# Performance work log

Measured on AMD Instinct MI355X. Metric: run time of the kernel, lower is better.

## Reference

```python
import jax, jax.numpy as jnp
import numpy as np

N, E, D_IN, H, D_OUT = 65536, 8, 90, 256, 4
MARGIN = 2.0  # boundary_margin
EPS = 1e-8


def setup_inputs() -> dict:
    key = jax.random.key(0)
    ks = jax.random.split(key, 6)
    return {
        "x": jax.random.normal(ks[0], (N, 3 + D_IN), dtype=jnp.float32),
        "centroids": jax.random.normal(ks[1], (E, 3), dtype=jnp.float32),
        "W1": jax.random.normal(ks[2], (E, D_IN, H), dtype=jnp.float32) * 0.05,
        "b1": jnp.zeros((E, H), dtype=jnp.float32),
        "W2": jax.random.normal(ks[3], (E, H, H), dtype=jnp.float32) * 0.05,
        "b2": jnp.zeros((E, H), dtype=jnp.float32),
        "W3": jax.random.normal(ks[4], (E, H, D_OUT), dtype=jnp.float32) * 0.05,
        "b3": jnp.zeros((E, D_OUT), dtype=jnp.float32),
    }


def _routing_weights(xyz, centroids):
    # torch.cdist(x[:, :3], centroids): Euclidean distance [N, E]
    diff = xyz[:, None, :] - centroids[None, :, :]
    d = jnp.sqrt(jnp.sum(diff * diff, axis=-1))
    inv = 1.0 / (d + EPS)
    dmin = jnp.min(d, axis=1, keepdims=True)
    inv = jnp.where(d > MARGIN * dmin, 0.0, inv)  # zero out far clusters
    return inv / jnp.sum(inv, axis=-1, keepdims=True)  # [N, E]


def reference(x, centroids, W1, b1, W2, b2, W3, b3):
    w = _routing_weights(x[:, :3], centroids)  # [N, E]
    feats = x[:, 3:]  # xyz_real=True -> experts see x[:, 3:]
    # Dense dispatch: evaluate every expert on all points, combine with weights.
    # Points masked out by routing have weight 0, so the math matches the
    # masked dispatch / weighted scatter-combine of the original module.
    h = jax.nn.relu(jnp.einsum('nd,edh->enh', feats, W1) + b1[:, None, :])
    h = jax.nn.relu(jnp.einsum('enh,ehk->enk', h, W2) + b2[:, None, :])
    out_e = jnp.einsum('enh,eho->eno', h, W3) + b3[:, None, :]  # [E, N, 4]
    return jnp.einsum('ne,eno->no', w, out_e)  # [N, 4]
```

## Files before the change

### kernel.cpp

```cpp
#include <hip/hip_runtime.h>


typedef __attribute__((ext_vector_type(8))) short   s16x8;
typedef __attribute__((ext_vector_type(4))) float   f32x4;

#define NPTS  65536
#define E_    8
#define DIN   90
#define H_    256
#define DOUT  4

#define W1P_ELEMS (E_*16*3*512)
#define W2P_ELEMS (E_*16*8*512)
#define W3P_ELEMS (E_*1*8*512)
#define W2P_OFF   (W1P_ELEMS)
#define W3P_OFF   (W1P_ELEMS + W2P_ELEMS)
#define WSP_TOTAL (W1P_ELEMS + W2P_ELEMS + W3P_ELEMS)
#define WSP_BYTES (WSP_TOTAL*2)
#define CNT_OFF   WSP_BYTES
#define LIST_OFF  (WSP_BYTES + 32)
#define XB_OFF    (LIST_OFF + E_*NPTS*2)
#define WL_OFF    (XB_OFF + (size_t)NPTS*96*2)

__device__ __forceinline__ unsigned short f2bf(float f) {
  union { float f; unsigned u; } v; v.f = f;
  unsigned u = v.u;
  u += 0x7fffu + ((u >> 16) & 1u);
  return (unsigned short)(u >> 16);
}
__device__ __forceinline__ unsigned pk2(float a, float b) {
  return (unsigned)f2bf(a) | ((unsigned)f2bf(b) << 16);
}

__global__ void prep_pack(const float* __restrict__ W1,
                          const float* __restrict__ W2,
                          const float* __restrict__ W3,
                          unsigned short* __restrict__ P) {
  int idx = blockIdx.x * blockDim.x + threadIdx.x;
  if (idx >= WSP_TOTAL) return;
  float val;
  if (idx < W2P_OFF) {
    int f = idx;
    int j = f & 7, l = (f >> 3) & 63, t = f >> 9;
    int ks = t % 3; t /= 3;
    int ct = t & 15, e = t >> 4;
    int k = ks*32 + (l>>4)*8 + j;
    int n = ct*16 + (l & 15);
    val = (k < DIN) ? W1[((size_t)e*DIN + k)*H_ + n] : 0.f;
  } else if (idx < W3P_OFF) {
    int f = idx - W2P_OFF;
    int j = f & 7, l = (f >> 3) & 63, t = f >> 9;
    int ks = t & 7; t >>= 3;
    int ct = t & 15, e = t >> 4;
    int k = ks*32 + (l>>4)*8 + j;
    int n = ct*16 + (l & 15);
    val = W2[((size_t)e*H_ + k)*H_ + n];
  } else {
    int f = idx - W3P_OFF;
    int j = f & 7, l = (f >> 3) & 63, t = f >> 9;
    int ks = t & 7, e = t >> 3;
    int k = ks*32 + (l>>4)*8 + j;
    int n = l & 15;
    val = (n < DOUT) ? W3[((size_t)e*H_ + k)*DOUT + n] : 0.f;
  }
  P[idx] = f2bf(val);
}

__global__ __launch_bounds__(256)
void x_pack(const float* __restrict__ x, unsigned* __restrict__ xb32) {
  int i = blockIdx.x * blockDim.x + threadIdx.x;
  if (i >= NPTS*48) return;
  int n = i / 48, c = i - n*48;
  const float* xr = x + (size_t)n*93 + 3;
  float v0 = (2*c   < DIN) ? xr[2*c]   : 0.f;
  float v1 = (2*c+1 < DIN) ? xr[2*c+1] : 0.f;
  xb32[(size_t)n*48 + c] = pk2(v0, v1);
}

__global__ __launch_bounds__(256)
void route_compact(const float* __restrict__ x,
                   const float* __restrict__ cen,
                   int* __restrict__ counts,
                   unsigned short* __restrict__ lists,
                   float* __restrict__ wlist) {
  const int tid = threadIdx.x;
  const int gid = blockIdx.x * 256 + tid;
  __shared__ int lcnt[E_], lbase[E_];
  if (tid < E_) lcnt[tid] = 0;
  __syncthreads();

  const float* xr = x + (size_t)gid*93;
  float px = xr[0], py = xr[1], pz = xr[2];
  float d[E_], dmin = 1e30f;
  #pragma unroll
  for (int e = 0; e < E_; e++) {
    float dx = px - cen[e*3+0], dy = py - cen[e*3+1], dz = pz - cen[e*3+2];
    d[e] = sqrtf(dx*dx + dy*dy + dz*dz);
    dmin = fminf(dmin, d[e]);
  }
  float inv[E_], s = 0.f;
  int act = 0;
  #pragma unroll
  for (int e = 0; e < E_; e++) {
    float iv = (d[e] > 2.0f*dmin) ? 0.f : 1.0f/(d[e] + 1e-8f);
    inv[e] = iv; s += iv;
    if (iv > 0.f) act |= (1 << e);
  }
  float rs = 1.0f/s;
  int myoff[E_];
  #pragma unroll
  for (int e = 0; e < E_; e++)
    if ((act >> e) & 1) myoff[e] = atomicAdd(&lcnt[e], 1);
  __syncthreads();
  if (tid < E_) lbase[tid] = atomicAdd(&counts[tid], lcnt[tid]);
  __syncthreads();
  #pragma unroll
  for (int e = 0; e < E_; e++)
    if ((act >> e) & 1) {
      int slot = e*NPTS + lbase[e] + myoff[e];
      lists[slot] = (unsigned short)gid;
      wlist[slot] = inv[e]*rs;
    }
}

__global__ __launch_bounds__(256, 3)
void expert_mlp(const float* __restrict__ b1,
                const float* __restrict__ b2,
                const float* __restrict__ b3,
                const unsigned short* __restrict__ P,
                const unsigned short* __restrict__ XB,
                const int* __restrict__ counts,
                const unsigned short* __restrict__ lists,
                const float* __restrict__ wlist,
                float* __restrict__ out) {
  const int e   = blockIdx.y;
  const int cnt = counts[e];
  const int t   = blockIdx.x;
  if (t*64 >= cnt) return;

  __shared__ __attribute__((aligned(16))) unsigned short sFb[64*128];
  __shared__ __attribute__((aligned(16))) unsigned short sH[64*256];

  const int tid  = threadIdx.x;
  const int wid  = tid >> 6;
  const int lane = tid & 63;
  const int lg   = lane >> 4;
  const int lr   = lane & 15;

  {
    int row  = tid >> 2;
    int slot = t*64 + row;
    int p    = (slot < cnt) ? (int)lists[e*NPTS + slot] : 0;
    const unsigned short* src = XB + (size_t)p*96;
    #pragma unroll
    for (int it = 0; it < 3; it++) {
      int chk = (tid & 3) + 4*it;
      s16x8 v = *(const s16x8*)(src + chk*8);
      int byt = (chk*16) ^ ((row & 7) << 4);
      *(s16x8*)((char*)sFb + row*256 + byt) = v;
    }
  }
  __syncthreads();

  f32x4 acc[4][4];
  #pragma unroll
  for (int nt = 0; nt < 4; nt++)
    #pragma unroll
    for (int bt = 0; bt < 4; bt++) acc[nt][bt] = (f32x4){0.f,0.f,0.f,0.f};

  {
    const unsigned short* PW1 = P + (((e*16 + wid*4)*3) << 9) + lane*8;
    #pragma unroll
    for (int ks = 0; ks < 3; ks++) {
      s16x8 bfr[4];
      #pragma unroll
      for (int bt = 0; bt < 4; bt++) {
        int m = 16*bt + lr;
        int byt = (64*ks + 16*lg) ^ ((m & 7) << 4);
        bfr[bt] = *(const s16x8*)((const char*)sFb + m*256 + byt);
      }
      #pragma unroll
      for (int nt = 0; nt < 4; nt++) {
        s16x8 a = *(const s16x8*)(PW1 + ((nt*3 + ks) << 9));
        #pragma unroll
        for (int bt = 0; bt < 4; bt++)
          acc[nt][bt] = __builtin_amdgcn_mfma_f32_16x16x32_bf16(a, bfr[bt], acc[nt][bt], 0,0,0);
      }
    }
  }

  #pragma unroll
  for (int nt = 0; nt < 4; nt++) {
    int ct = wid*4 + nt;
    float4 bv = *(const float4*)&b1[e*H_ + ct*16 + lg*4];
    #pragma unroll
    for (int bt = 0; bt < 4; bt++) {
      float v0 = fmaxf(acc[nt][bt][0] + bv.x, 0.f);
      float v1 = fmaxf(acc[nt][bt][1] + bv.y, 0.f);
      float v2 = fmaxf(acc[nt][bt][2] + bv.z, 0.f);
      float v3 = fmaxf(acc[nt][bt][3] + bv.w, 0.f);
      int m   = 16*bt + lr;
      int byt = (32*ct + 8*lg) ^ ((m & 7) << 4);
      uint2 pkd; pkd.x = pk2(v0, v1); pkd.y = pk2(v2, v3);
      *(uint2*)((char*)sH + m*512 + byt) = pkd;
    }
  }
  __syncthreads();

  #pragma unroll
  for (int nt = 0; nt < 4; nt++)
    #pragma unroll
    for (int bt = 0; bt < 4; bt++) acc[nt][bt] = (f32x4){0.f,0.f,0.f,0.f};

  {
    const unsigned short* PW2 = P + W2P_OFF + (((e*16 + wid*4)*8) << 9) + lane*8;
    #pragma unroll
    for (int ks = 0; ks < 8; ks++) {
      s16x8 bfr[4];
      #pragma unroll
      for (int bt = 0; bt < 4; bt++) {
        int m = 16*bt + lr;
        int byt = (64*ks + 16*lg) ^ ((m & 7) << 4);
        bfr[bt] = *(const s16x8*)((const char*)sH + m*512 + byt);
      }
      #pragma unroll
      for (int nt = 0; nt < 4; nt++) {
        s16x8 a = *(const s16x8*)(PW2 + ((nt*8 + ks) << 9));
        #pragma unroll
        for (int bt = 0; bt < 4; bt++)
          acc[nt][bt] = __builtin_amdgcn_mfma_f32_16x16x32_bf16(a, bfr[bt], acc[nt][bt], 0,0,0);
      }
    }
  }
  __syncthreads();

  #pragma unroll
  for (int nt = 0; nt < 4; nt++) {
    int ct = wid*4 + nt;
    float4 bv = *(const float4*)&b2[e*H_ + ct*16 + lg*4];
    #pragma unroll
    for (int bt = 0; bt < 4; bt++) {
      float v0 = fmaxf(acc[nt][bt][0] + bv.x, 0.f);
      float v1 = fmaxf(acc[nt][bt][1] + bv.y, 0.f);
      float v2 = fmaxf(acc[nt][bt][2] + bv.z, 0.f);
      float v3 = fmaxf(acc[nt][bt][3] + bv.w, 0.f);
      int m   = 16*bt + lr;
      int byt = (32*ct + 8*lg) ^ ((m & 7) << 4);
      uint2 pkd; pkd.x = pk2(v0, v1); pkd.y = pk2(v2, v3);
      *(uint2*)((char*)sH + m*512 + byt) = pkd;
    }
  }
  __syncthreads();

  f32x4 acc3 = (f32x4){0.f,0.f,0.f,0.f};
  #pragma unroll
  for (int ks = 0; ks < 8; ks++) {
    int m = 16*wid + lr;
    int byt = (64*ks + 16*lg) ^ ((m & 7) << 4);
    s16x8 bb = *(const s16x8*)((const char*)sH + m*512 + byt);
    s16x8 a  = *(const s16x8*)(P + W3P_OFF + ((e*8 + ks) << 9) + lane*8);
    acc3 = __builtin_amdgcn_mfma_f32_16x16x32_bf16(a, bb, acc3, 0,0,0);
  }

  if (lg == 0) {
    int slot = t*64 + 16*wid + lr;
    float wv = (slot < cnt) ? wlist[e*NPTS + slot] : 0.f;
    if (wv != 0.f) {
      int p = (int)lists[e*NPTS + slot];
      #pragma unroll
      for (int r = 0; r < 4; r++)
        atomicAdd(&out[(size_t)p*DOUT + r], wv * (acc3[r] + b3[e*DOUT + r]));
    }
  }
}

extern "C" void kernel_launch(void* const* d_in, const int* in_sizes, int n_in,
                              void* d_out, int out_size, void* d_ws, size_t ws_size,
                              hipStream_t stream) {
  const float* x   = (const float*)d_in[0];
  const float* cen = (const float*)d_in[1];
  const float* W1  = (const float*)d_in[2];
  const float* b1  = (const float*)d_in[3];
  const float* W2  = (const float*)d_in[4];
  const float* b2  = (const float*)d_in[5];
  const float* W3  = (const float*)d_in[6];
  const float* b3  = (const float*)d_in[7];

  unsigned short* P     = (unsigned short*)d_ws;
  int*            cnts  = (int*)((char*)d_ws + CNT_OFF);
  unsigned short* lists = (unsigned short*)((char*)d_ws + LIST_OFF);
  unsigned short* XB    = (unsigned short*)((char*)d_ws + XB_OFF);
  float*          WL    = (float*)((char*)d_ws + WL_OFF);
  float* out = (float*)d_out;

  (void)hipMemsetAsync(cnts, 0, 32, stream);
  (void)hipMemsetAsync(out, 0, (size_t)NPTS*DOUT*sizeof(float), stream);
  prep_pack<<<dim3((WSP_TOTAL + 255)/256), dim3(256), 0, stream>>>(W1, W2, W3, P);
  x_pack<<<dim3((NPTS*48 + 255)/256), dim3(256), 0, stream>>>(x, (unsigned*)XB);
  route_compact<<<dim3(NPTS/256), dim3(256), 0, stream>>>(x, cen, cnts, lists, WL);
  expert_mlp<<<dim3(NPTS/64, E_), dim3(256), 0, stream>>>(b1, b2, b3, P, XB,
                                                          cnts, lists, WL, out);
}
```

Baseline: 101.9 us.

## Make expert MLP persistent with a flat tile schedule and prefetch next tile

Replaces the 2D grid over (tiles, experts), where most blocks exited early, with a fixed grid of 768 persistent blocks. Each block walks a contiguous range of a flattened tile index across all experts. While layer 2 runs, the block prefetches the next tile's input rows into registers and writes them to shared memory once the current tile no longer needs it. The two memsets are also folded into the prep_pack and x_pack kernels. This cuts launch and early-exit overhead and hides gather latency, at the cost of an extra barrier per tile, higher register pressure, and possible load imbalance when the total tile count is not a multiple of the grid.

```diff
diff --git a/kernel.cpp b/kernel.cpp
--- a/kernel.cpp
+++ b/kernel.cpp
@@ -9,6 +9,7 @@
 #define DIN   90
 #define H_    256
 #define DOUT  4
+#define GRID_ 768
 
 #define W1P_ELEMS (E_*16*3*512)
 #define W2P_ELEMS (E_*16*8*512)
@@ -35,8 +36,10 @@
 __global__ void prep_pack(const float* __restrict__ W1,
                           const float* __restrict__ W2,
                           const float* __restrict__ W3,
-                          unsigned short* __restrict__ P) {
+                          unsigned short* __restrict__ P,
+                          int* __restrict__ cnts) {
   int idx = blockIdx.x * blockDim.x + threadIdx.x;
+  if (idx < E_) cnts[idx] = 0;
   if (idx >= WSP_TOTAL) return;
   float val;
   if (idx < W2P_OFF) {
@@ -67,8 +70,10 @@
 }
 
 __global__ __launch_bounds__(256)
-void x_pack(const float* __restrict__ x, unsigned* __restrict__ xb32) {
+void x_pack(const float* __restrict__ x, unsigned* __restrict__ xb32,
+            float* __restrict__ out) {
   int i = blockIdx.x * blockDim.x + threadIdx.x;
+  if (i < NPTS*DOUT) out[i] = 0.f;
   if (i >= NPTS*48) return;
   int n = i / 48, c = i - n*48;
   const float* xr = x + (size_t)n*93 + 3;
@@ -133,11 +138,6 @@
                 const unsigned short* __restrict__ lists,
                 const float* __restrict__ wlist,
                 float* __restrict__ out) {
-  const int e   = blockIdx.y;
-  const int cnt = counts[e];
-  const int t   = blockIdx.x;
-  if (t*64 >= cnt) return;
-
   __shared__ __attribute__((aligned(16))) unsigned short sFb[64*128];
   __shared__ __attribute__((aligned(16))) unsigned short sH[64*256];
 
@@ -147,130 +147,176 @@
   const int lg   = lane >> 4;
   const int lr   = lane & 15;
 
+  int toff[E_+1]; toff[0] = 0;
+  int cnte[E_];
+  #pragma unroll
+  for (int e = 0; e < E_; e++) {
+    cnte[e] = counts[e];
+    toff[e+1] = toff[e] + ((cnte[e] + 63) >> 6);
+  }
+  const int total = toff[E_];
+  const int bid   = blockIdx.x;
+  const int wg    = (bid & 7) * (GRID_ >> 3) + (bid >> 3);
+  const int chunk = (total + GRID_ - 1) / GRID_;
+  const int start = wg * chunk;
+  const int end   = min(start + chunk, total);
+  if (start >= end) return;
+
+  const int srow = tid >> 2;
+
   {
-    int row  = tid >> 2;
-    int slot = t*64 + row;
-    int p    = (slot < cnt) ? (int)lists[e*NPTS + slot] : 0;
+    int e0 = 0; { int g = start; while (g >= toff[e0+1]) ++e0; }
+    int t0 = start - toff[e0];
+    int slot = t0*64 + srow;
+    int p    = (slot < cnte[e0]) ? (int)lists[e0*NPTS + slot] : 0;
     const unsigned short* src = XB + (size_t)p*96;
     #pragma unroll
     for (int it = 0; it < 3; it++) {
       int chk = (tid & 3) + 4*it;
       s16x8 v = *(const s16x8*)(src + chk*8);
-      int byt = (chk*16) ^ ((row & 7) << 4);
-      *(s16x8*)((char*)sFb + row*256 + byt) = v;
+      int byt = (chk*16) ^ ((srow & 7) << 4);
+      *(s16x8*)((char*)sFb + srow*256 + byt) = v;
     }
   }
   __syncthreads();
 
-  f32x4 acc[4][4];
-  #pragma unroll
-  for (int nt = 0; nt < 4; nt++)
-    #pragma unroll
-    for (int bt = 0; bt < 4; bt++) acc[nt][bt] = (f32x4){0.f,0.f,0.f,0.f};
-
-  {
-    const unsigned short* PW1 = P + (((e*16 + wid*4)*3) << 9) + lane*8;
-    #pragma unroll
-    for (int ks = 0; ks < 3; ks++) {
-      s16x8 bfr[4];
+  int e = 0; { int g = start; while (g >= toff[e+1]) ++e; }
+
+  for (int g = start; g < end; ++g) {
+    while (g >= toff[e+1]) ++e;
+    const int t   = g - toff[e];
+    const int cnt = cnte[e];
+
+    f32x4 acc[4][4];
+    #pragma unroll
+    for (int nt = 0; nt < 4; nt++)
+      #pragma unroll
+      for (int bt = 0; bt < 4; bt++) acc[nt][bt] = (f32x4){0.f,0.f,0.f,0.f};
+    {
+      const unsigned short* PW1 = P + (((e*16 + wid*4)*3) << 9) + lane*8;
+      #pragma unroll
+      for (int ks = 0; ks < 3; ks++) {
+        s16x8 bfr[4];
+        #pragma unroll
+        for (int bt = 0; bt < 4; bt++) {
+          int m = 16*bt + lr;
+          int byt = (64*ks + 16*lg) ^ ((m & 7) << 4);
+          bfr[bt] = *(const s16x8*)((const char*)sFb + m*256 + byt);
+        }
+        #pragma unroll
+        for (int nt = 0; nt < 4; nt++) {
+          s16x8 a = *(const s16x8*)(PW1 + ((nt*3 + ks) << 9));
+          #pragma unroll
+          for (int bt = 0; bt < 4; bt++)
+            acc[nt][bt] = __builtin_amdgcn_mfma_f32_16x16x32_bf16(a, bfr[bt], acc[nt][bt], 0,0,0);
+        }
+      }
+    }
+    #pragma unroll
+    for (int nt = 0; nt < 4; nt++) {
+      int ct = wid*4 + nt;
+      float4 bv = *(const float4*)&b1[e*H_ + ct*16 + lg*4];
       #pragma unroll
       for (int bt = 0; bt < 4; bt++) {
-        int m = 16*bt + lr;
-        int byt = (64*ks + 16*lg) ^ ((m & 7) << 4);
-        bfr[bt] = *(const s16x8*)((const char*)sFb + m*256 + byt);
-      }
-      #pragma unroll
-      for (int nt = 0; nt < 4; nt++) {
-        s16x8 a = *(const s16x8*)(PW1 + ((nt*3 + ks) << 9));
-        #pragma unroll
-        for (int bt = 0; bt < 4; bt++)
-          acc[nt][bt] = __builtin_amdgcn_mfma_f32_16x16x32_bf16(a, bfr[bt], acc[nt][bt], 0,0,0);
-      }
-    }
-  }
-
-  #pragma unroll
-  for (int nt = 0; nt < 4; nt++) {
-    int ct = wid*4 + nt;
-    float4 bv = *(const float4*)&b1[e*H_ + ct*16 + lg*4];
-    #pragma unroll
-    for (int bt = 0; bt < 4; bt++) {
-      float v0 = fmaxf(acc[nt][bt][0] + bv.x, 0.f);
-      float v1 = fmaxf(acc[nt][bt][1] + bv.y, 0.f);
-      float v2 = fmaxf(acc[nt][bt][2] + bv.z, 0.f);
-      float v3 = fmaxf(acc[nt][bt][3] + bv.w, 0.f);
-      int m   = 16*bt + lr;
-      int byt = (32*ct + 8*lg) ^ ((m & 7) << 4);
-      uint2 pkd; pkd.x = pk2(v0, v1); pkd.y = pk2(v2, v3);
-      *(uint2*)((char*)sH + m*512 + byt) = pkd;
-    }
-  }
-  __syncthreads();
-
-  #pragma unroll
-  for (int nt = 0; nt < 4; nt++)
-    #pragma unroll
-    for (int bt = 0; bt < 4; bt++) acc[nt][bt] = (f32x4){0.f,0.f,0.f,0.f};
-
-  {
-    const unsigned short* PW2 = P + W2P_OFF + (((e*16 + wid*4)*8) << 9) + lane*8;
+        float v0 = fmaxf(acc[nt][bt][0] + bv.x, 0.f);
+        float v1 = fmaxf(acc[nt][bt][1] + bv.y, 0.f);
+        float v2 = fmaxf(acc[nt][bt][2] + bv.z, 0.f);
+        float v3 = fmaxf(acc[nt][bt][3] + bv.w, 0.f);
+        int m   = 16*bt + lr;
+        int byt = (32*ct + 8*lg) ^ ((m & 7) << 4);
+        uint2 pkd; pkd.x = pk2(v0, v1); pkd.y = pk2(v2, v3);
+        *(uint2*)((char*)sH + m*512 + byt) = pkd;
+      }
+    }
+    __syncthreads();
+
+    const bool havenext = (g + 1 < end);
+    s16x8 stg0, stg1, stg2;
+    if (havenext) {
+      int e2 = e; while (g+1 >= toff[e2+1]) ++e2;
+      int t2 = g + 1 - toff[e2];
+      int slot2 = t2*64 + srow;
+      int p2    = (slot2 < cnte[e2]) ? (int)lists[e2*NPTS + slot2] : 0;
+      const unsigned short* src = XB + (size_t)p2*96;
+      stg0 = *(const s16x8*)(src + ((tid & 3) + 0)*8);
+      stg1 = *(const s16x8*)(src + ((tid & 3) + 4)*8);
+      stg2 = *(const s16x8*)(src + ((tid & 3) + 8)*8);
+    }
+
+    #pragma unroll
+    for (int nt = 0; nt < 4; nt++)
+      #pragma unroll
+      for (int bt = 0; bt < 4; bt++) acc[nt][bt] = (f32x4){0.f,0.f,0.f,0.f};
+    {
+      const unsigned short* PW2 = P + W2P_OFF + (((e*16 + wid*4)*8) << 9) + lane*8;
+      #pragma unroll
+      for (int ks = 0; ks < 8; ks++) {
+        s16x8 bfr[4];
+        #pragma unroll
+        for (int bt = 0; bt < 4; bt++) {
+          int m = 16*bt + lr;
+          int byt = (64*ks + 16*lg) ^ ((m & 7) << 4);
+          bfr[bt] = *(const s16x8*)((const char*)sH + m*512 + byt);
+        }
+        #pragma unroll
+        for (int nt = 0; nt < 4; nt++) {
+          s16x8 a = *(const s16x8*)(PW2 + ((nt*8 + ks) << 9));
+          #pragma unroll
+          for (int bt = 0; bt < 4; bt++)
+            acc[nt][bt] = __builtin_amdgcn_mfma_f32_16x16x32_bf16(a, bfr[bt], acc[nt][bt], 0,0,0);
+        }
+      }
+    }
+    __syncthreads();
+
+    #pragma unroll
+    for (int nt = 0; nt < 4; nt++) {
+      int ct = wid*4 + nt;
+      float4 bv = *(const float4*)&b2[e*H_ + ct*16 + lg*4];
+      #pragma unroll
+      for (int bt = 0; bt < 4; bt++) {
+        float v0 = fmaxf(acc[nt][bt][0] + bv.x, 0.f);
+        float v1 = fmaxf(acc[nt][bt][1] + bv.y, 0.f);
+        float v2 = fmaxf(acc[nt][bt][2] + bv.z, 0.f);
+        float v3 = fmaxf(acc[nt][bt][3] + bv.w, 0.f);
+        int m   = 16*bt + lr;
+        int byt = (32*ct + 8*lg) ^ ((m & 7) << 4);
+        uint2 pkd; pkd.x = pk2(v0, v1); pkd.y = pk2(v2, v3);
+        *(uint2*)((char*)sH + m*512 + byt) = pkd;
+      }
+    }
+    __syncthreads();
+
+    if (havenext) {
+      int chk0 = tid & 3;
+      int b0 = ((chk0    )*16) ^ ((srow & 7) << 4);
+      int b1_ = ((chk0 + 4)*16) ^ ((srow & 7) << 4);
+      int b2_ = ((chk0 + 8)*16) ^ ((srow & 7) << 4);
+      *(s16x8*)((char*)sFb + srow*256 + b0)  = stg0;
+      *(s16x8*)((char*)sFb + srow*256 + b1_) = stg1;
+      *(s16x8*)((char*)sFb + srow*256 + b2_) = stg2;
+    }
+
+    f32x4 acc3 = (f32x4){0.f,0.f,0.f,0.f};
     #pragma unroll
     for (int ks = 0; ks < 8; ks++) {
-      s16x8 bfr[4];
-      #pragma unroll
-      for (int bt = 0; bt < 4; bt++) {
-        int m = 16*bt + lr;
-        int byt = (64*ks + 16*lg) ^ ((m & 7) << 4);
-        bfr[bt] = *(const s16x8*)((const char*)sH + m*512 + byt);
-      }
-      #pragma unroll
-      for (int nt = 0; nt < 4; nt++) {
-        s16x8 a = *(const s16x8*)(PW2 + ((nt*8 + ks) << 9));
-        #pragma unroll
-        for (int bt = 0; bt < 4; bt++)
-          acc[nt][bt] = __builtin_amdgcn_mfma_f32_16x16x32_bf16(a, bfr[bt], acc[nt][bt], 0,0,0);
-      }
-    }
-  }
-  __syncthreads();
-
-  #pragma unroll
-  for (int nt = 0; nt < 4; nt++) {
-    int ct = wid*4 + nt;
-    float4 bv = *(const float4*)&b2[e*H_ + ct*16 + lg*4];
-    #pragma unroll
-    for (int bt = 0; bt < 4; bt++) {
-      float v0 = fmaxf(acc[nt][bt][0] + bv.x, 0.f);
-      float v1 = fmaxf(acc[nt][bt][1] + bv.y, 0.f);
-      float v2 = fmaxf(acc[nt][bt][2] + bv.z, 0.f);
-      float v3 = fmaxf(acc[nt][bt][3] + bv.w, 0.f);
-      int m   = 16*bt + lr;
-      int byt = (32*ct + 8*lg) ^ ((m & 7) << 4);
-      uint2 pkd; pkd.x = pk2(v0, v1); pkd.y = pk2(v2, v3);
-      *(uint2*)((char*)sH + m*512 + byt) = pkd;
-    }
-  }
-  __syncthreads();
-
-  f32x4 acc3 = (f32x4){0.f,0.f,0.f,0.f};
-  #pragma unroll
-  for (int ks = 0; ks < 8; ks++) {
-    int m = 16*wid + lr;
-    int byt = (64*ks + 16*lg) ^ ((m & 7) << 4);
-    s16x8 bb = *(const s16x8*)((const char*)sH + m*512 + byt);
-    s16x8 a  = *(const s16x8*)(P + W3P_OFF + ((e*8 + ks) << 9) + lane*8);
-    acc3 = __builtin_amdgcn_mfma_f32_16x16x32_bf16(a, bb, acc3, 0,0,0);
-  }
-
-  if (lg == 0) {
-    int slot = t*64 + 16*wid + lr;
-    float wv = (slot < cnt) ? wlist[e*NPTS + slot] : 0.f;
-    if (wv != 0.f) {
-      int p = (int)lists[e*NPTS + slot];
-      #pragma unroll
-      for (int r = 0; r < 4; r++)
-        atomicAdd(&out[(size_t)p*DOUT + r], wv * (acc3[r] + b3[e*DOUT + r]));
-    }
+      int m = 16*wid + lr;
+      int byt = (64*ks + 16*lg) ^ ((m & 7) << 4);
+      s16x8 bb = *(const s16x8*)((const char*)sH + m*512 + byt);
+      s16x8 a  = *(const s16x8*)(P + W3P_OFF + ((e*8 + ks) << 9) + lane*8);
+      acc3 = __builtin_amdgcn_mfma_f32_16x16x32_bf16(a, bb, acc3, 0,0,0);
+    }
+    if (lg == 0) {
+      int slot = t*64 + 16*wid + lr;
+      float wv = (slot < cnt) ? wlist[e*NPTS + slot] : 0.f;
+      if (wv != 0.f) {
+        int p = (int)lists[e*NPTS + slot];
+        #pragma unroll
+        for (int r = 0; r < 4; r++)
+          atomicAdd(&out[(size_t)p*DOUT + r], wv * (acc3[r] + b3[e*DOUT + r]));
+      }
+    }
+    __syncthreads();
   }
 }
 
@@ -293,11 +339,9 @@
   float*          WL    = (float*)((char*)d_ws + WL_OFF);
   float* out = (float*)d_out;
 
-  (void)hipMemsetAsync(cnts, 0, 32, stream);
-  (void)hipMemsetAsync(out, 0, (size_t)NPTS*DOUT*sizeof(float), stream);
-  prep_pack<<<dim3((WSP_TOTAL + 255)/256), dim3(256), 0, stream>>>(W1, W2, W3, P);
-  x_pack<<<dim3((NPTS*48 + 255)/256), dim3(256), 0, stream>>>(x, (unsigned*)XB);
+  prep_pack<<<dim3((WSP_TOTAL + 255)/256), dim3(256), 0, stream>>>(W1, W2, W3, P, cnts);
+  x_pack<<<dim3((NPTS*48 + 255)/256), dim3(256), 0, stream>>>(x, (unsigned*)XB, out);
   route_compact<<<dim3(NPTS/256), dim3(256), 0, stream>>>(x, cen, cnts, lists, WL);
-  expert_mlp<<<dim3(NPTS/64, E_), dim3(256), 0, stream>>>(b1, b2, b3, P, XB,
-                                                          cnts, lists, WL, out);
-}
+  expert_mlp<<<dim3(GRID_), dim3(256), 0, stream>>>(b1, b2, b3, P, XB,
+                                                    cnts, lists, WL, out);
+}
```

Result: slower. 130.4 us (+27.9%).

## Fuse weight pack, x pack, routing and output zeroing into one launch

Applied to the files above, without the earlier changes.

Merges the three preprocessing kernels and the output memset into a single kernel that picks its role from the block index, removing two launches and one memset along with their inter-kernel gaps. The expert MLP epilogue also swaps the software round-to-nearest bf16 packing for the hardware v_cvt_pk_bf16_f32 instruction to cut ALU work. The fused kernel's routing branch uses __syncthreads only inside its own branch, which is uniform per block, and output zeroing now rides along in the x-pack blocks.

```diff
diff --git a/kernel.cpp b/kernel.cpp
--- a/kernel.cpp
+++ b/kernel.cpp
@@ -22,6 +22,10 @@
 #define XB_OFF    (LIST_OFF + E_*NPTS*2)
 #define WL_OFF    (XB_OFF + (size_t)NPTS*96*2)
 
+#define PREP_BLKS (WSP_TOTAL/256)
+#define XPK_BLKS  (NPTS*48/256)
+#define RC_BLKS   (NPTS/256)
+
 __device__ __forceinline__ unsigned short f2bf(float f) {
   union { float f; unsigned u; } v; v.f = f;
   unsigned u = v.u;
@@ -31,96 +35,104 @@
 __device__ __forceinline__ unsigned pk2(float a, float b) {
   return (unsigned)f2bf(a) | ((unsigned)f2bf(b) << 16);
 }
-
-__global__ void prep_pack(const float* __restrict__ W1,
-                          const float* __restrict__ W2,
-                          const float* __restrict__ W3,
-                          unsigned short* __restrict__ P) {
-  int idx = blockIdx.x * blockDim.x + threadIdx.x;
-  if (idx >= WSP_TOTAL) return;
-  float val;
-  if (idx < W2P_OFF) {
-    int f = idx;
-    int j = f & 7, l = (f >> 3) & 63, t = f >> 9;
-    int ks = t % 3; t /= 3;
-    int ct = t & 15, e = t >> 4;
-    int k = ks*32 + (l>>4)*8 + j;
-    int n = ct*16 + (l & 15);
-    val = (k < DIN) ? W1[((size_t)e*DIN + k)*H_ + n] : 0.f;
-  } else if (idx < W3P_OFF) {
-    int f = idx - W2P_OFF;
-    int j = f & 7, l = (f >> 3) & 63, t = f >> 9;
-    int ks = t & 7; t >>= 3;
-    int ct = t & 15, e = t >> 4;
-    int k = ks*32 + (l>>4)*8 + j;
-    int n = ct*16 + (l & 15);
-    val = W2[((size_t)e*H_ + k)*H_ + n];
+__device__ __forceinline__ unsigned cvtpk(float a, float b) {
+  unsigned r;
+  asm("v_cvt_pk_bf16_f32 %0, %1, %2" : "=v"(r) : "v"(a), "v"(b));
+  return r;
+}
+
+__global__ __launch_bounds__(256)
+void fused_prep(const float* __restrict__ x,
+                const float* __restrict__ cen,
+                const float* __restrict__ W1,
+                const float* __restrict__ W2,
+                const float* __restrict__ W3,
+                unsigned short* __restrict__ P,
+                unsigned* __restrict__ xb32,
+                float* __restrict__ out,
+                int* __restrict__ counts,
+                unsigned short* __restrict__ lists,
+                float* __restrict__ wlist) {
+  const int b   = blockIdx.x;
+  const int tid = threadIdx.x;
+
+  if (b < PREP_BLKS) {
+    int idx = b*256 + tid;
+    float val;
+    if (idx < W2P_OFF) {
+      int f = idx;
+      int j = f & 7, l = (f >> 3) & 63, t = f >> 9;
+      int ks = t % 3; t /= 3;
+      int ct = t & 15, e = t >> 4;
+      int k = ks*32 + (l>>4)*8 + j;
+      int n = ct*16 + (l & 15);
+      val = (k < DIN) ? W1[((size_t)e*DIN + k)*H_ + n] : 0.f;
+    } else if (idx < W3P_OFF) {
+      int f = idx - W2P_OFF;
+      int j = f & 7, l = (f >> 3) & 63, t = f >> 9;
+      int ks = t & 7; t >>= 3;
+      int ct = t & 15, e = t >> 4;
+      int k = ks*32 + (l>>4)*8 + j;
+      int n = ct*16 + (l & 15);
+      val = W2[((size_t)e*H_ + k)*H_ + n];
+    } else {
+      int f = idx - W3P_OFF;
+      int j = f & 7, l = (f >> 3) & 63, t = f >> 9;
+      int ks = t & 7, e = t >> 3;
+      int k = ks*32 + (l>>4)*8 + j;
+      int n = l & 15;
+      val = (n < DOUT) ? W3[((size_t)e*H_ + k)*DOUT + n] : 0.f;
+    }
+    P[idx] = f2bf(val);
+
+  } else if (b < PREP_BLKS + XPK_BLKS) {
+    int i = (b - PREP_BLKS)*256 + tid;
+    if (i < NPTS*DOUT) out[i] = 0.f;
+    int n = i / 48, c = i - n*48;
+    const float* xr = x + (size_t)n*93 + 3;
+    float v0 = (2*c   < DIN) ? xr[2*c]   : 0.f;
+    float v1 = (2*c+1 < DIN) ? xr[2*c+1] : 0.f;
+    xb32[(size_t)n*48 + c] = pk2(v0, v1);
+
   } else {
-    int f = idx - W3P_OFF;
-    int j = f & 7, l = (f >> 3) & 63, t = f >> 9;
-    int ks = t & 7, e = t >> 3;
-    int k = ks*32 + (l>>4)*8 + j;
-    int n = l & 15;
-    val = (n < DOUT) ? W3[((size_t)e*H_ + k)*DOUT + n] : 0.f;
-  }
-  P[idx] = f2bf(val);
-}
-
-__global__ __launch_bounds__(256)
-void x_pack(const float* __restrict__ x, unsigned* __restrict__ xb32) {
-  int i = blockIdx.x * blockDim.x + threadIdx.x;
-  if (i >= NPTS*48) return;
-  int n = i / 48, c = i - n*48;
-  const float* xr = x + (size_t)n*93 + 3;
-  float v0 = (2*c   < DIN) ? xr[2*c]   : 0.f;
-  float v1 = (2*c+1 < DIN) ? xr[2*c+1] : 0.f;
-  xb32[(size_t)n*48 + c] = pk2(v0, v1);
-}
-
-__global__ __launch_bounds__(256)
-void route_compact(const float* __restrict__ x,
-                   const float* __restrict__ cen,
-                   int* __restrict__ counts,
-                   unsigned short* __restrict__ lists,
-                   float* __restrict__ wlist) {
-  const int tid = threadIdx.x;
-  const int gid = blockIdx.x * 256 + tid;
-  __shared__ int lcnt[E_], lbase[E_];
-  if (tid < E_) lcnt[tid] = 0;
-  __syncthreads();
-
-  const float* xr = x + (size_t)gid*93;
-  float px = xr[0], py = xr[1], pz = xr[2];
-  float d[E_], dmin = 1e30f;
-  #pragma unroll
-  for (int e = 0; e < E_; e++) {
-    float dx = px - cen[e*3+0], dy = py - cen[e*3+1], dz = pz - cen[e*3+2];
-    d[e] = sqrtf(dx*dx + dy*dy + dz*dz);
-    dmin = fminf(dmin, d[e]);
-  }
-  float inv[E_], s = 0.f;
-  int act = 0;
-  #pragma unroll
-  for (int e = 0; e < E_; e++) {
-    float iv = (d[e] > 2.0f*dmin) ? 0.f : 1.0f/(d[e] + 1e-8f);
-    inv[e] = iv; s += iv;
-    if (iv > 0.f) act |= (1 << e);
-  }
-  float rs = 1.0f/s;
-  int myoff[E_];
-  #pragma unroll
-  for (int e = 0; e < E_; e++)
-    if ((act >> e) & 1) myoff[e] = atomicAdd(&lcnt[e], 1);
-  __syncthreads();
-  if (tid < E_) lbase[tid] = atomicAdd(&counts[tid], lcnt[tid]);
-  __syncthreads();
-  #pragma unroll
-  for (int e = 0; e < E_; e++)
-    if ((act >> e) & 1) {
-      int slot = e*NPTS + lbase[e] + myoff[e];
-      lists[slot] = (unsigned short)gid;
-      wlist[slot] = inv[e]*rs;
-    }
+    int gid = (b - PREP_BLKS - XPK_BLKS)*256 + tid;
+    __shared__ int lcnt[E_], lbase[E_];
+    if (tid < E_) lcnt[tid] = 0;
+    __syncthreads();
+
+    const float* xr = x + (size_t)gid*93;
+    float px = xr[0], py = xr[1], pz = xr[2];
+    float d[E_], dmin = 1e30f;
+    #pragma unroll
+    for (int e = 0; e < E_; e++) {
+      float dx = px - cen[e*3+0], dy = py - cen[e*3+1], dz = pz - cen[e*3+2];
+      d[e] = sqrtf(dx*dx + dy*dy + dz*dz);
+      dmin = fminf(dmin, d[e]);
+    }
+    float inv[E_], s = 0.f;
+    int act = 0;
+    #pragma unroll
+    for (int e = 0; e < E_; e++) {
+      float iv = (d[e] > 2.0f*dmin) ? 0.f : 1.0f/(d[e] + 1e-8f);
+      inv[e] = iv; s += iv;
+      if (iv > 0.f) act |= (1 << e);
+    }
+    float rs = 1.0f/s;
+    int myoff[E_];
+    #pragma unroll
+    for (int e = 0; e < E_; e++)
+      if ((act >> e) & 1) myoff[e] = atomicAdd(&lcnt[e], 1);
+    __syncthreads();
+    if (tid < E_) lbase[tid] = atomicAdd(&counts[tid], lcnt[tid]);
+    __syncthreads();
+    #pragma unroll
+    for (int e = 0; e < E_; e++)
+      if ((act >> e) & 1) {
+        int slot = e*NPTS + lbase[e] + myoff[e];
+        lists[slot] = (unsigned short)gid;
+        wlist[slot] = inv[e]*rs;
+      }
+  }
 }
 
 __global__ __launch_bounds__(256, 3)
@@ -201,7 +213,7 @@
       float v3 = fmaxf(acc[nt][bt][3] + bv.w, 0.f);
       int m   = 16*bt + lr;
       int byt = (32*ct + 8*lg) ^ ((m & 7) << 4);
-      uint2 pkd; pkd.x = pk2(v0, v1); pkd.y = pk2(v2, v3);
+      uint2 pkd; pkd.x = cvtpk(v0, v1); pkd.y = cvtpk(v2, v3);
       *(uint2*)((char*)sH + m*512 + byt) = pkd;
     }
   }
@@ -246,7 +258,7 @@
       float v3 = fmaxf(acc[nt][bt][3] + bv.w, 0.f);
       int m   = 16*bt + lr;
       int byt = (32*ct + 8*lg) ^ ((m & 7) << 4);
-      uint2 pkd; pkd.x = pk2(v0, v1); pkd.y = pk2(v2, v3);
+      uint2 pkd; pkd.x = cvtpk(v0, v1); pkd.y = cvtpk(v2, v3);
       *(uint2*)((char*)sH + m*512 + byt) = pkd;
     }
   }
@@ -294,10 +306,8 @@
   float* out = (float*)d_out;
 
   (void)hipMemsetAsync(cnts, 0, 32, stream);
-  (void)hipMemsetAsync(out, 0, (size_t)NPTS*DOUT*sizeof(float), stream);
-  prep_pack<<<dim3((WSP_TOTAL + 255)/256), dim3(256), 0, stream>>>(W1, W2, W3, P);
-  x_pack<<<dim3((NPTS*48 + 255)/256), dim3(256), 0, stream>>>(x, (unsigned*)XB);
-  route_compact<<<dim3(NPTS/256), dim3(256), 0, stream>>>(x, cen, cnts, lists, WL);
+  fused_prep<<<dim3(PREP_BLKS + XPK_BLKS + RC_BLKS), dim3(256), 0, stream>>>(
+      x, cen, W1, W2, W3, P, (unsigned*)XB, out, cnts, lists, WL);
   expert_mlp<<<dim3(NPTS/64, E_), dim3(256), 0, stream>>>(b1, b2, b3, P, XB,
                                                           cnts, lists, WL, out);
 }
```

New measurement: 120.9 us. 1.19x slower.
